# Optimization experiments

Measured on AMD Instinct MI355X. Metric: run time of the kernel, lower is better.

Reference implementation:

```python
import jax, jax.numpy as jnp
import numpy as np

NUM_CHANNELS = 4096  # fill_max for ch_ids; all ids appear w.h.p. since batch >> channels


def setup_inputs() -> dict:
    key = jax.random.key(0)
    k1, k2, k3 = jax.random.split(key, 3)
    B, D = 524288, 128
    z = jax.random.normal(k1, (B, D), dtype=jnp.float32)
    y = jax.random.randint(k2, (B,), 0, 2, dtype=jnp.int64)
    ch_ids = jax.random.randint(k3, (B,), 0, NUM_CHANNELS, dtype=jnp.int64)
    return {"z": z, "y": y, "ch_ids": ch_ids}


def reference(z, y, ch_ids):
    # Segment-mean of z over channel ids, plus first-occurrence label per channel.
    C = NUM_CHANNELS
    B = z.shape[0]
    seg = ch_ids.astype(jnp.int32)
    # sum and count per channel in a single pass each (scatter-add)
    z_sum = jax.ops.segment_sum(z, seg, num_segments=C)              # (C, D)
    cnt = jax.ops.segment_sum(jnp.ones((B,), z.dtype), seg, num_segments=C)  # (C,)
    z_ch = z_sum / jnp.maximum(cnt, 1.0)[:, None]  # mean reduction
    # label of first window in each channel: scatter-min of row indices, then gather
    first_idx = jnp.full((C,), B, dtype=jnp.int32).at[seg].min(jnp.arange(B, dtype=jnp.int32))
    y_ch = y[jnp.minimum(first_idx, B - 1)]
    return z_ch, y_ch
```

## Files before the change

### kernel.cpp

```cpp
#include <hip/hip_runtime.h>

#define C_CH 4096
#define D_DIM 128

typedef float f32x2 __attribute__((ext_vector_type(2)));

__global__ __launch_bounds__(256) void init_kernel(int* cnt, int* first, int B) {
    int i = blockIdx.x * blockDim.x + threadIdx.x;
    if (i < C_CH) { cnt[i] = 0; first[i] = B - 1; }
}

__global__ __launch_bounds__(256) void count_kernel(const int* __restrict__ ids,
                                                    int* cnt, int* first, int B) {
    int t = blockIdx.x * blockDim.x + threadIdx.x;
    int row = t * 4;
    if (row + 3 < B) {
        int4 v = ((const int4*)ids)[t];
        atomicAdd(&cnt[v.x], 1); atomicMin(&first[v.x], row + 0);
        atomicAdd(&cnt[v.y], 1); atomicMin(&first[v.y], row + 1);
        atomicAdd(&cnt[v.z], 1); atomicMin(&first[v.z], row + 2);
        atomicAdd(&cnt[v.w], 1); atomicMin(&first[v.w], row + 3);
    } else {
        for (int k = 0; k < 4; ++k)
            if (row + k < B) { int c = ids[row + k]; atomicAdd(&cnt[c], 1); atomicMin(&first[c], row + k); }
    }
}

__global__ void scan_kernel(const int* __restrict__ cnt, int* offs, int* cursor) {
    __shared__ int wtot[16];
    int tid  = threadIdx.x;
    int lane = tid & 63;
    int wave = tid >> 6;
    int base = tid * 4;
    int v0 = cnt[base + 0], v1 = cnt[base + 1], v2 = cnt[base + 2], v3 = cnt[base + 3];
    int s = v0 + v1 + v2 + v3;
    int inc = s;
    for (int off = 1; off < 64; off <<= 1) {
        int n = __shfl_up(inc, off, 64);
        if (lane >= off) inc += n;
    }
    if (lane == 63) wtot[wave] = inc;
    __syncthreads();
    if (wave == 0) {
        int t = (lane < 16) ? wtot[lane] : 0;
        int ts = t;
        for (int off = 1; off < 16; off <<= 1) {
            int n = __shfl_up(ts, off, 64);
            if (lane >= off) ts += n;
        }
        if (lane < 16) wtot[lane] = ts - t;
    }
    __syncthreads();
    int run = wtot[wave] + (inc - s);
    offs[base + 0] = run; cursor[base + 0] = run; run += v0;
    offs[base + 1] = run; cursor[base + 1] = run; run += v1;
    offs[base + 2] = run; cursor[base + 2] = run; run += v2;
    offs[base + 3] = run; cursor[base + 3] = run; run += v3;
    if (tid == 1023) offs[C_CH] = run;
}

__global__ __launch_bounds__(256) void scatter_kernel(const int* __restrict__ ids,
                                                      int* cursor, int* order, int B) {
    int t = blockIdx.x * blockDim.x + threadIdx.x;
    int row = t * 4;
    if (row + 3 < B) {
        int4 v = ((const int4*)ids)[t];
        int p0 = atomicAdd(&cursor[v.x], 1);
        int p1 = atomicAdd(&cursor[v.y], 1);
        int p2 = atomicAdd(&cursor[v.z], 1);
        int p3 = atomicAdd(&cursor[v.w], 1);
        __builtin_nontemporal_store(row + 0, &order[p0]);
        __builtin_nontemporal_store(row + 1, &order[p1]);
        __builtin_nontemporal_store(row + 2, &order[p2]);
        __builtin_nontemporal_store(row + 3, &order[p3]);
    } else {
        for (int k = 0; k < 4; ++k)
            if (row + k < B) { int pos = atomicAdd(&cursor[ids[row + k]], 1); order[pos] = row + k; }
    }
}

__global__ __launch_bounds__(256) void reduce_kernel(
        const float* __restrict__ z, const int* __restrict__ order,
        const int* __restrict__ offs, const int* __restrict__ first,
        const int* __restrict__ y, float* __restrict__ out, int B) {
    int w = blockIdx.x * 4 + (threadIdx.x >> 6);
    int lane = threadIdx.x & 63;
    if (w >= C_CH) return;
    int beg = offs[w], end = offs[w + 1];
    const f32x2* z2 = (const f32x2*)z;

    f32x2 a0 = {0.f, 0.f}, a1 = {0.f, 0.f}, a2 = {0.f, 0.f}, a3 = {0.f, 0.f};
    f32x2 a4 = {0.f, 0.f}, a5 = {0.f, 0.f}, a6 = {0.f, 0.f}, a7 = {0.f, 0.f};

    if (end > beg) {
        int idx[16];
        #pragma unroll
        for (int k = 0; k < 16; ++k)
            idx[k] = order[min(beg + k, end - 1)];
        for (int r = beg; r < end; r += 16) {
            f32x2 v[16];
            #pragma unroll
            for (int k = 0; k < 16; ++k)
                v[k] = __builtin_nontemporal_load(&z2[(size_t)idx[k] * 64 + lane]);
            int rn = r + 16;
            if (rn < end) {
                #pragma unroll
                for (int k = 0; k < 16; ++k)
                    idx[k] = order[min(rn + k, end - 1)];
            }
            #pragma unroll
            for (int k = 0; k < 16; ++k) {
                if (r + k < end) {
                    switch (k & 7) {
                        case 0: a0 += v[k]; break;
                        case 1: a1 += v[k]; break;
                        case 2: a2 += v[k]; break;
                        case 3: a3 += v[k]; break;
                        case 4: a4 += v[k]; break;
                        case 5: a5 += v[k]; break;
                        case 6: a6 += v[k]; break;
                        case 7: a7 += v[k]; break;
                    }
                }
            }
        }
    }
    f32x2 sum = ((a0 + a1) + (a2 + a3)) + ((a4 + a5) + (a6 + a7));
    int cnt_c = end - beg;
    float inv = 1.f / (float)max(cnt_c, 1);
    f32x2 res; res.x = sum.x * inv; res.y = sum.y * inv;
    ((f32x2*)out)[(size_t)w * 64 + lane] = res;
    if (lane == 0) {
        out[(size_t)C_CH * D_DIM + w] = (float)y[min(first[w], B - 1)];
    }
}

extern "C" void kernel_launch(void* const* d_in, const int* in_sizes, int n_in,
                              void* d_out, int out_size, void* d_ws, size_t ws_size,
                              hipStream_t stream) {
    const float* z   = (const float*)d_in[0];
    const int*   y   = (const int*)d_in[1];
    const int*   ids = (const int*)d_in[2];
    float* out = (float*)d_out;
    const int B = in_sizes[2];

    int* cnt    = (int*)d_ws;
    int* offs   = cnt + C_CH;
    int* cursor = offs + C_CH + 4;
    int* first  = cursor + C_CH;
    int* order  = first + C_CH;

    init_kernel<<<(C_CH + 255) / 256, 256, 0, stream>>>(cnt, first, B);
    int tquads = (B + 3) / 4;
    count_kernel<<<(tquads + 255) / 256, 256, 0, stream>>>(ids, cnt, first, B);
    scan_kernel<<<1, 1024, 0, stream>>>(cnt, offs, cursor);
    scatter_kernel<<<(tquads + 255) / 256, 256, 0, stream>>>(ids, cursor, order, B);
    reduce_kernel<<<C_CH / 4, 256, 0, stream>>>(z, order, offs, first, y, out, B);
}
```

Baseline: 429.6 us.

## Fuse five-kernel segment-mean pipeline into one cooperative kernel with grid syncs

Replaces the separate init, count, scan, scatter and reduce launches with one cooperative kernel of 512 blocks that uses grid-wide syncs between phases and grid-stride loops. The scan is now done by a single 256-thread block handling 16 counts per thread. The aim is to remove per-launch overhead and inter-kernel gaps. In exchange the reduce phase runs on a fixed grid of 2048 waves looping over 4096 channels, which may lower memory-level parallelism, and grid syncs add their own cost.

After: 655.7 us. 1.53x slower.

```diff
diff --git a/kernel.cpp b/kernel.cpp
--- a/kernel.cpp
+++ b/kernel.cpp
@@ -1,70 +1,71 @@
 #include <hip/hip_runtime.h>
+#include <hip/hip_cooperative_groups.h>
 
 #define C_CH 4096
 #define D_DIM 128
+#define GRID 512
+#define BLOCK 256
+#define NTHREADS (GRID * BLOCK)
+
+namespace cg = cooperative_groups;
 
 typedef float f32x2 __attribute__((ext_vector_type(2)));
 
-__global__ __launch_bounds__(256) void init_kernel(int* cnt, int* first, int B) {
-    int i = blockIdx.x * blockDim.x + threadIdx.x;
-    if (i < C_CH) { cnt[i] = 0; first[i] = B - 1; }
-}
+__global__ __launch_bounds__(BLOCK) void fused_pipeline(
+        const float* __restrict__ z, const int* __restrict__ y,
+        const int* __restrict__ ids, float* __restrict__ out,
+        int* cnt, int* offs, int* cursor, int* first, int* order, int B) {
+    cg::grid_group grid = cg::this_grid();
+    const int tid  = threadIdx.x;
+    const int gtid = blockIdx.x * BLOCK + tid;
+    const int nquads = B >> 2;
+    const int4* ids4 = (const int4*)ids;
 
-__global__ __launch_bounds__(256) void count_kernel(const int* __restrict__ ids,
-                                                    int* cnt, int* first, int B) {
-    int t = blockIdx.x * blockDim.x + threadIdx.x;
-    int row = t * 4;
-    if (row + 3 < B) {
-        int4 v = ((const int4*)ids)[t];
+    if (gtid < C_CH) { cnt[gtid] = 0; first[gtid] = B - 1; }
+    grid.sync();
+
+    for (int q = gtid; q < nquads; q += NTHREADS) {
+        int4 v = ids4[q];
+        int row = q << 2;
         atomicAdd(&cnt[v.x], 1); atomicMin(&first[v.x], row + 0);
         atomicAdd(&cnt[v.y], 1); atomicMin(&first[v.y], row + 1);
         atomicAdd(&cnt[v.z], 1); atomicMin(&first[v.z], row + 2);
         atomicAdd(&cnt[v.w], 1); atomicMin(&first[v.w], row + 3);
-    } else {
-        for (int k = 0; k < 4; ++k)
-            if (row + k < B) { int c = ids[row + k]; atomicAdd(&cnt[c], 1); atomicMin(&first[c], row + k); }
     }
-}
+    for (int i = (nquads << 2) + gtid; i < B; i += NTHREADS) {
+        int c = ids[i];
+        atomicAdd(&cnt[c], 1); atomicMin(&first[c], i);
+    }
+    grid.sync();
 
-__global__ void scan_kernel(const int* __restrict__ cnt, int* offs, int* cursor) {
-    __shared__ int wtot[16];
-    int tid  = threadIdx.x;
-    int lane = tid & 63;
-    int wave = tid >> 6;
-    int base = tid * 4;
-    int v0 = cnt[base + 0], v1 = cnt[base + 1], v2 = cnt[base + 2], v3 = cnt[base + 3];
-    int s = v0 + v1 + v2 + v3;
-    int inc = s;
-    for (int off = 1; off < 64; off <<= 1) {
-        int n = __shfl_up(inc, off, 64);
-        if (lane >= off) inc += n;
+    if (blockIdx.x == 0) {
+        __shared__ int wsum[4];
+        int lane = tid & 63, wv = tid >> 6;
+        int base = tid * 16;
+        int v[16]; int s = 0;
+        #pragma unroll
+        for (int k = 0; k < 16; ++k) { v[k] = cnt[base + k]; s += v[k]; }
+        int inc = s;
+        for (int off = 1; off < 64; off <<= 1) {
+            int n = __shfl_up(inc, off, 64);
+            if (lane >= off) inc += n;
+        }
+        if (lane == 63) wsum[wv] = inc;
+        __syncthreads();
+        int wbase = 0;
+        for (int i = 0; i < wv; ++i) wbase += wsum[i];
+        int run = wbase + (inc - s);
+        #pragma unroll
+        for (int k = 0; k < 16; ++k) {
+            offs[base + k] = run; cursor[base + k] = run; run += v[k];
+        }
+        if (tid == BLOCK - 1) offs[C_CH] = run;
     }
-    if (lane == 63) wtot[wave] = inc;
-    __syncthreads();
-    if (wave == 0) {
-        int t = (lane < 16) ? wtot[lane] : 0;
-        int ts = t;
-        for (int off = 1; off < 16; off <<= 1) {
-            int n = __shfl_up(ts, off, 64);
-            if (lane >= off) ts += n;
-        }
-        if (lane < 16) wtot[lane] = ts - t;
-    }
-    __syncthreads();
-    int run = wtot[wave] + (inc - s);
-    offs[base + 0] = run; cursor[base + 0] = run; run += v0;
-    offs[base + 1] = run; cursor[base + 1] = run; run += v1;
-    offs[base + 2] = run; cursor[base + 2] = run; run += v2;
-    offs[base + 3] = run; cursor[base + 3] = run; run += v3;
-    if (tid == 1023) offs[C_CH] = run;
-}
+    grid.sync();
 
-__global__ __launch_bounds__(256) void scatter_kernel(const int* __restrict__ ids,
-                                                      int* cursor, int* order, int B) {
-    int t = blockIdx.x * blockDim.x + threadIdx.x;
-    int row = t * 4;
-    if (row + 3 < B) {
-        int4 v = ((const int4*)ids)[t];
+    for (int q = gtid; q < nquads; q += NTHREADS) {
+        int4 v = ids4[q];
+        int row = q << 2;
         int p0 = atomicAdd(&cursor[v.x], 1);
         int p1 = atomicAdd(&cursor[v.y], 1);
         int p2 = atomicAdd(&cursor[v.z], 1);
@@ -73,65 +74,60 @@
         __builtin_nontemporal_store(row + 1, &order[p1]);
         __builtin_nontemporal_store(row + 2, &order[p2]);
         __builtin_nontemporal_store(row + 3, &order[p3]);
-    } else {
-        for (int k = 0; k < 4; ++k)
-            if (row + k < B) { int pos = atomicAdd(&cursor[ids[row + k]], 1); order[pos] = row + k; }
     }
-}
+    for (int i = (nquads << 2) + gtid; i < B; i += NTHREADS) {
+        int pos = atomicAdd(&cursor[ids[i]], 1);
+        order[pos] = i;
+    }
+    grid.sync();
 
-__global__ __launch_bounds__(256) void reduce_kernel(
-        const float* __restrict__ z, const int* __restrict__ order,
-        const int* __restrict__ offs, const int* __restrict__ first,
-        const int* __restrict__ y, float* __restrict__ out, int B) {
-    int w = blockIdx.x * 4 + (threadIdx.x >> 6);
-    int lane = threadIdx.x & 63;
-    if (w >= C_CH) return;
-    int beg = offs[w], end = offs[w + 1];
     const f32x2* z2 = (const f32x2*)z;
-
-    f32x2 a0 = {0.f, 0.f}, a1 = {0.f, 0.f}, a2 = {0.f, 0.f}, a3 = {0.f, 0.f};
-    f32x2 a4 = {0.f, 0.f}, a5 = {0.f, 0.f}, a6 = {0.f, 0.f}, a7 = {0.f, 0.f};
-
-    if (end > beg) {
-        int idx[16];
-        #pragma unroll
-        for (int k = 0; k < 16; ++k)
-            idx[k] = order[min(beg + k, end - 1)];
-        for (int r = beg; r < end; r += 16) {
-            f32x2 v[16];
+    const int lane = tid & 63;
+    const int waveGlobal = (blockIdx.x << 2) + (tid >> 6);
+    for (int w = waveGlobal; w < C_CH; w += GRID * (BLOCK / 64)) {
+        int beg = offs[w], end = offs[w + 1];
+        f32x2 a0 = {0.f,0.f}, a1 = {0.f,0.f}, a2 = {0.f,0.f}, a3 = {0.f,0.f};
+        f32x2 a4 = {0.f,0.f}, a5 = {0.f,0.f}, a6 = {0.f,0.f}, a7 = {0.f,0.f};
+        if (end > beg) {
+            int idx[16];
             #pragma unroll
             for (int k = 0; k < 16; ++k)
-                v[k] = __builtin_nontemporal_load(&z2[(size_t)idx[k] * 64 + lane]);
-            int rn = r + 16;
-            if (rn < end) {
+                idx[k] = order[min(beg + k, end - 1)];
+            for (int r = beg; r < end; r += 16) {
+                f32x2 v[16];
                 #pragma unroll
                 for (int k = 0; k < 16; ++k)
-                    idx[k] = order[min(rn + k, end - 1)];
-            }
-            #pragma unroll
-            for (int k = 0; k < 16; ++k) {
-                if (r + k < end) {
-                    switch (k & 7) {
-                        case 0: a0 += v[k]; break;
-                        case 1: a1 += v[k]; break;
-                        case 2: a2 += v[k]; break;
-                        case 3: a3 += v[k]; break;
-                        case 4: a4 += v[k]; break;
-                        case 5: a5 += v[k]; break;
-                        case 6: a6 += v[k]; break;
-                        case 7: a7 += v[k]; break;
+                    v[k] = __builtin_nontemporal_load(&z2[(size_t)idx[k] * 64 + lane]);
+                int rn = r + 16;
+                if (rn < end) {
+                    #pragma unroll
+                    for (int k = 0; k < 16; ++k)
+                        idx[k] = order[min(rn + k, end - 1)];
+                }
+                #pragma unroll
+                for (int k = 0; k < 16; ++k) {
+                    if (r + k < end) {
+                        switch (k & 7) {
+                            case 0: a0 += v[k]; break;
+                            case 1: a1 += v[k]; break;
+                            case 2: a2 += v[k]; break;
+                            case 3: a3 += v[k]; break;
+                            case 4: a4 += v[k]; break;
+                            case 5: a5 += v[k]; break;
+                            case 6: a6 += v[k]; break;
+                            case 7: a7 += v[k]; break;
+                        }
                     }
                 }
             }
         }
-    }
-    f32x2 sum = ((a0 + a1) + (a2 + a3)) + ((a4 + a5) + (a6 + a7));
-    int cnt_c = end - beg;
-    float inv = 1.f / (float)max(cnt_c, 1);
-    f32x2 res; res.x = sum.x * inv; res.y = sum.y * inv;
-    ((f32x2*)out)[(size_t)w * 64 + lane] = res;
-    if (lane == 0) {
-        out[(size_t)C_CH * D_DIM + w] = (float)y[min(first[w], B - 1)];
+        f32x2 sum = ((a0 + a1) + (a2 + a3)) + ((a4 + a5) + (a6 + a7));
+        float inv = 1.f / (float)max(end - beg, 1);
+        f32x2 res; res.x = sum.x * inv; res.y = sum.y * inv;
+        ((f32x2*)out)[(size_t)w * 64 + lane] = res;
+        if (lane == 0) {
+            out[(size_t)C_CH * D_DIM + w] = (float)y[min(first[w], B - 1)];
+        }
     }
 }
 
@@ -142,7 +138,7 @@
     const int*   y   = (const int*)d_in[1];
     const int*   ids = (const int*)d_in[2];
     float* out = (float*)d_out;
-    const int B = in_sizes[2];
+    int B = in_sizes[2];
 
     int* cnt    = (int*)d_ws;
     int* offs   = cnt + C_CH;
@@ -150,10 +146,9 @@
     int* first  = cursor + C_CH;
     int* order  = first + C_CH;
 
-    init_kernel<<<(C_CH + 255) / 256, 256, 0, stream>>>(cnt, first, B);
-    int tquads = (B + 3) / 4;
-    count_kernel<<<(tquads + 255) / 256, 256, 0, stream>>>(ids, cnt, first, B);
-    scan_kernel<<<1, 1024, 0, stream>>>(cnt, offs, cursor);
-    scatter_kernel<<<(tquads + 255) / 256, 256, 0, stream>>>(ids, cursor, order, B);
-    reduce_kernel<<<C_CH / 4, 256, 0, stream>>>(z, order, offs, first, y, out, B);
+    void* args[] = {(void*)&z, (void*)&y, (void*)&ids, (void*)&out,
+                    (void*)&cnt, (void*)&offs, (void*)&cursor, (void*)&first,
+                    (void*)&order, (void*)&B};
+    hipLaunchCooperativeKernel((void*)fused_pipeline, dim3(GRID), dim3(BLOCK),
+                               args, 0, stream);
 }
```
